# Performance work log

Measured on AMD Instinct MI355X. Metric: run time of the kernel, lower is better.

Reference implementation:

```python
import jax, jax.numpy as jnp
import numpy as np

B, E, D, T, R = 8192, 4096, 256, 128, 4
K = 64                # dkn_n_neighbors
TAU_SQ = 4.0          # tau**2
EMB_SCALE = 0.07      # keeps sq-dists ~2.5 so exp(-d2) weights are meaningful
LOG_BASE = -27.6310211159
EPS = 1e-12


def _rev_cumsum(a, axis):
    # flip -> cumsum -> flip, as in torch .flip().cumsum().flip()
    return jnp.flip(jnp.cumsum(jnp.flip(a, axis), axis), axis)


def _kernel_weights(x, ex):
    # exact KNN stand-in for the ANN index: squared L2 distances [B, E]
    d2 = (jnp.sum(x * x, axis=1, keepdims=True)
          + jnp.sum(ex * ex, axis=1)[None, :]
          - 2.0 * (x @ ex.T))
    neg_d2, idx = jax.lax.top_k(-d2, K)          # k nearest per query
    sq = jnp.maximum(-neg_d2, 0.0)               # [B, K]
    vals = jnp.exp(-sq) * (sq <= TAU_SQ).astype(x.dtype)
    rows = jnp.arange(x.shape[0])[:, None]       # [B, 1]
    # sparse exp-distance weights scattered into dense [B, E]
    return jnp.zeros((x.shape[0], ex.shape[0]), x.dtype).at[rows, idx].set(vals)


def setup_inputs() -> dict:
    key = jax.random.key(0)
    k0, k1, k2, k3 = jax.random.split(key, 4)
    x = jax.random.normal(k0, (B, D), dtype=jnp.float32) * EMB_SCALE
    ex = jax.random.normal(k1, (E, D), dtype=jnp.float32) * EMB_SCALE
    log_ev = jax.random.normal(k2, (E, T, R), dtype=jnp.float32) - 2.0
    log_cen = jax.random.normal(k3, (E, T), dtype=jnp.float32) - 2.0
    log_b_ev = jnp.full((T, R), LOG_BASE, dtype=jnp.float32)
    log_b_cen = jnp.full((T,), LOG_BASE, dtype=jnp.float32)
    return {
        "x": x,
        "exemplar_embeddings": ex,
        "log_exemplar_event_counts": log_ev,
        "log_exemplar_censor_counts": log_cen,
        "log_baseline_event_counts": log_b_ev,
        "log_baseline_censor_counts": log_b_cen,
    }


def reference(x, exemplar_embeddings, log_exemplar_event_counts,
              log_exemplar_censor_counts, log_baseline_event_counts,
              log_baseline_censor_counts):
    kw = _kernel_weights(x, exemplar_embeddings)             # [B, E]

    b_ev = jnp.exp(log_baseline_event_counts)                # [T, R]
    b_cen = jnp.exp(log_baseline_censor_counts)              # [T]
    b_at_risk = _rev_cumsum(b_ev.sum(1) + b_cen, 0)          # [T]

    ev = jnp.exp(log_exemplar_event_counts)                  # [E, T, R]
    cen = jnp.exp(log_exemplar_censor_counts)                # [E, T]
    at_risk = _rev_cumsum(ev.sum(2) + cen, 1)                # [E, T]

    denom = kw @ at_risk + b_at_risk[None, :] + EPS          # [B, T]
    numer = jnp.einsum('be,etr->btr', kw, ev) + b_ev[None]   # [B, T, R]

    esh = jnp.clip(numer / denom[..., None], EPS, 1.0 - EPS) # [B, T, R]
    event_specific_hazards = jnp.moveaxis(esh, -1, 0)        # [R, B, T]
    overall = jnp.clip(numer.sum(-1) / denom, EPS, 1.0 - EPS)  # [B, T]
    return event_specific_hazards, overall
```

## Files before the change

kernel.cpp:

```cpp
#include <hip/hip_runtime.h>
#include <hip/hip_fp16.h>
#include <math.h>

namespace {

constexpr int NB = 8192;
constexpr int NE = 4096;
constexpr int ND = 256;
constexpr int NT = 128;
constexpr int NR = 4;
constexpr int NK = 64;
constexpr int NCAND = 320;
constexpr float TAUSQ = 4.0f;
constexpr float FEPS = 1e-12f;
constexpr float QS = 256.0f / 4.5f;

typedef short s16x8 __attribute__((ext_vector_type(8)));
typedef float f32x4 __attribute__((ext_vector_type(4)));

__device__ __forceinline__ unsigned short f2bf_rne(float f) {
  unsigned int u = __float_as_uint(f);
  unsigned int r = (u + 0x7FFFu + ((u >> 16) & 1u)) >> 16;
  return (unsigned short)r;
}
__device__ __forceinline__ unsigned short f2h(float f) {
  return __half_as_ushort(__float2half(f));
}
__device__ __forceinline__ float h2f(unsigned short s) {
  return __half2float(__ushort_as_half(s));
}

__device__ __forceinline__ void gl_lds16(const void* g, void* lds) {
  __builtin_amdgcn_global_load_lds(
      (const __attribute__((address_space(1))) unsigned int*)g,
      (__attribute__((address_space(3))) unsigned int*)lds, 16, 0, 0);
}

__global__ void k_prep_base(const float* __restrict__ lbev, const float* __restrict__ lbcen,
                            float* __restrict__ bev, float* __restrict__ bar) {
  __shared__ float s[NT];
  int t = threadIdx.x;
  float acc = expf(lbcen[t]);
  for (int r = 0; r < NR; ++r) {
    float v = expf(lbev[t * NR + r]);
    bev[t * NR + r] = v;
    acc += v;
  }
  s[t] = acc;
  __syncthreads();
  float su = 0.f;
  for (int u = t; u < NT; ++u) su += s[u];
  bar[t] = su;
}

__global__ void k_prep_ev(const float* __restrict__ lev, const float* __restrict__ lcen,
                          unsigned short* __restrict__ EVh, unsigned short* __restrict__ ARh) {
  __shared__ float s[NT];
  int e = blockIdx.x, t = threadIdx.x;
  float acc = expf(lcen[(size_t)e * NT + t]);
  const float* src = lev + ((size_t)e * NT + t) * NR;
  float o0 = expf(src[0]), o1 = expf(src[1]), o2 = expf(src[2]), o3 = expf(src[3]);
  ushort4 h4;
  h4.x = f2h(o0); h4.y = f2h(o1); h4.z = f2h(o2); h4.w = f2h(o3);
  *reinterpret_cast<ushort4*>(EVh + ((size_t)e * NT + t) * NR) = h4;
  acc += o0 + o1 + o2 + o3;
  s[t] = acc;
  __syncthreads();
  float su = 0.f;
  for (int u = t; u < NT; ++u) su += s[u];
  ARh[(size_t)e * NT + t] = f2h(su);
}

__global__ void k_split(const float* __restrict__ x, const float* __restrict__ ex,
                        unsigned short* __restrict__ xh, unsigned short* __restrict__ eh,
                        float* __restrict__ xn, float* __restrict__ exn) {
  int row = blockIdx.x, l = threadIdx.x;
  bool isx = row < NB;
  const float* p = isx ? (x + (size_t)row * ND) : (ex + (size_t)(row - NB) * ND);
  unsigned short* dst = isx ? (xh + (size_t)row * ND) : (eh + (size_t)(row - NB) * ND);
  float4 v = reinterpret_cast<const float4*>(p)[l];
  float nv = v.x * v.x + v.y * v.y + v.z * v.z + v.w * v.w;
  ushort4 h4;
  h4.x = f2bf_rne(v.x); h4.y = f2bf_rne(v.y);
  h4.z = f2bf_rne(v.z); h4.w = f2bf_rne(v.w);
  reinterpret_cast<ushort4*>(dst)[l] = h4;
  for (int o = 32; o > 0; o >>= 1) nv += __shfl_down(nv, o);
  if (l == 0) { if (isx) xn[row] = nv; else exn[row - NB] = nv; }
}

__global__ __launch_bounds__(256) void k_dist_mfma(
    const unsigned short* __restrict__ xh, const unsigned short* __restrict__ eh,
    const float* __restrict__ xn, const float* __restrict__ exn,
    unsigned char* __restrict__ d2q) {
  __shared__ __align__(16) unsigned char As[128 * 64];
  __shared__ __align__(16) unsigned char Bs[128 * 64];
  int tid = threadIdx.x;
  int l = tid & 63, w = tid >> 6;
  int wr = w >> 1, wc = w & 1;
  int nb = blockIdx.x * 128, mb = blockIdx.y * 128;

  f32x4 acc[4][4];
  #pragma unroll
  for (int m = 0; m < 4; ++m)
    #pragma unroll
    for (int n = 0; n < 4; ++n)
      acc[m][n] = (f32x4){0.f, 0.f, 0.f, 0.f};

  for (int k0 = 0; k0 < ND; k0 += 32) {
    #pragma unroll
    for (int h = 0; h < 2; ++h) {
      int c = h * 256 + tid;
      int row = c >> 2, slot = c & 3;
      int swz = (row ^ (row >> 2)) & 3;
      int gcol = k0 + ((slot ^ swz) << 3);
      gl_lds16(xh + (size_t)(mb + row) * ND + gcol, As + c * 16);
      gl_lds16(eh + (size_t)(nb + row) * ND + gcol, Bs + c * 16);
    }
    __syncthreads();
    s16x8 af[4], bf_[4];
    int ko = l >> 4;
    #pragma unroll
    for (int m = 0; m < 4; ++m) {
      int r = wr * 64 + m * 16 + (l & 15);
      int swz = (r ^ (r >> 2)) & 3;
      af[m] = *(const s16x8*)(As + r * 64 + ((ko ^ swz) << 4));
    }
    #pragma unroll
    for (int n = 0; n < 4; ++n) {
      int r = wc * 64 + n * 16 + (l & 15);
      int swz = (r ^ (r >> 2)) & 3;
      bf_[n] = *(const s16x8*)(Bs + r * 64 + ((ko ^ swz) << 4));
    }
    #pragma unroll
    for (int m = 0; m < 4; ++m)
      #pragma unroll
      for (int n = 0; n < 4; ++n)
        acc[m][n] = __builtin_amdgcn_mfma_f32_16x16x32_bf16(af[m], bf_[n], acc[m][n], 0, 0, 0);
    __syncthreads();
  }

  int col0 = nb + wc * 64 + (l & 15);
  int row0 = mb + wr * 64 + (l >> 4) * 4;
  float exnv[4];
  #pragma unroll
  for (int n = 0; n < 4; ++n) exnv[n] = exn[col0 + n * 16];
  #pragma unroll
  for (int m = 0; m < 4; ++m) {
    #pragma unroll
    for (int j = 0; j < 4; ++j) {
      int qrow = row0 + m * 16 + j;
      float xq = xn[qrow];
      #pragma unroll
      for (int n = 0; n < 4; ++n) {
        float d2 = xq + exnv[n] - 2.f * acc[m][n][j];
        int bin = (int)floorf(d2 * QS);
        bin = bin < 0 ? 0 : (bin > 255 ? 255 : bin);
        d2q[(size_t)qrow * NE + (col0 + n * 16)] = (unsigned char)bin;
      }
    }
  }
}

__global__ __launch_bounds__(256, 8) void k_select(
    const unsigned char* __restrict__ d2q,
    const float* __restrict__ x, const float* __restrict__ ex,
    const float* __restrict__ xn, const float* __restrict__ exn,
    float* __restrict__ selw, int* __restrict__ seli) {
  __shared__ unsigned int hist[256];
  __shared__ float4 xs[64];
  __shared__ int cand_e[NCAND];
  __shared__ float cand_d[NCAND];
  __shared__ unsigned int wsum[4];
  __shared__ int s_cb, s_nc;

  int tid = threadIdx.x;
  int l = tid & 63, w = tid >> 6;
  int b = blockIdx.x;

  uint4 rb = reinterpret_cast<const uint4*>(d2q + (size_t)b * NE)[tid];
  if (tid < 64) xs[tid] = reinterpret_cast<const float4*>(x + (size_t)b * ND)[tid];
  hist[tid] = 0u;
  __syncthreads();

  unsigned int wd[4] = {rb.x, rb.y, rb.z, rb.w};
  #pragma unroll
  for (int c = 0; c < 4; ++c)
    #pragma unroll
    for (int k = 0; k < 4; ++k)
      atomicAdd(&hist[(wd[c] >> (8 * k)) & 255u], 1u);
  __syncthreads();

  if (w == 0) {
    unsigned int h0 = hist[l * 4], h1 = hist[l * 4 + 1], h2 = hist[l * 4 + 2], h3 = hist[l * 4 + 3];
    unsigned int gs = h0 + h1 + h2 + h3;
    unsigned int sc = gs;
    #pragma unroll
    for (int o = 1; o < 64; o <<= 1) { unsigned int v = __shfl_up(sc, o); if (l >= o) sc += v; }
    unsigned int excl = sc - gs;
    unsigned int c0 = excl + h0, c1 = c0 + h1, c2 = c1 + h2, c3 = c2 + h3;
    int local = (c0 >= (unsigned)NK) ? 0 : (c1 >= (unsigned)NK) ? 1
              : (c2 >= (unsigned)NK) ? 2 : (c3 >= (unsigned)NK) ? 3 : -1;
    unsigned long long ball = __ballot(local >= 0);
    int first = __ffsll((long long)ball) - 1;
    if (l == first) s_cb = l * 4 + local;
  }
  __syncthreads();
  int cbg = s_cb < 255 ? s_cb + 1 : 255;

  int myc = 0;
  #pragma unroll
  for (int c = 0; c < 4; ++c)
    #pragma unroll
    for (int k = 0; k < 4; ++k)
      myc += ((int)((wd[c] >> (8 * k)) & 255u) <= cbg) ? 1 : 0;
  int sc = myc;
  #pragma unroll
  for (int o = 1; o < 64; o <<= 1) { int v = __shfl_up(sc, o); if (l >= o) sc += v; }
  if (l == 63) wsum[w] = (unsigned)sc;
  __syncthreads();
  int base = 0;
  for (int i = 0; i < w; ++i) base += (int)wsum[i];
  int slot = base + sc - myc;
  #pragma unroll
  for (int c = 0; c < 4; ++c)
    #pragma unroll
    for (int k = 0; k < 4; ++k) {
      int bin = (int)((wd[c] >> (8 * k)) & 255u);
      if (bin <= cbg) {
        if (slot < NCAND) cand_e[slot] = tid * 16 + c * 4 + k;
        ++slot;
      }
    }
  if (tid == 255) s_nc = (base + sc) < NCAND ? (base + sc) : NCAND;
  __syncthreads();

  int nc = s_nc;
  float bxn = xn[b];
  int g = tid >> 4, gj = tid & 15;
  for (int c = g; c < nc; c += 16) {
    int e = cand_e[c];
    const float4* ep = reinterpret_cast<const float4*>(ex + (size_t)e * ND);
    float s = 0.f;
    #pragma unroll
    for (int it = 0; it < 4; ++it) {
      float4 xv = xs[gj + 16 * it];
      float4 evv = ep[gj + 16 * it];
      s += xv.x * evv.x + xv.y * evv.y + xv.z * evv.z + xv.w * evv.w;
    }
    s += __shfl_xor(s, 1, 16);
    s += __shfl_xor(s, 2, 16);
    s += __shfl_xor(s, 4, 16);
    s += __shfl_xor(s, 8, 16);
    if (gj == 0) cand_d[c] = bxn + exn[e] - 2.f * s;
  }
  __syncthreads();

  for (int i = tid; i < nc; i += 256) {
    float di = cand_d[i];
    int rank = 0;
    for (int j = 0; j < nc; ++j) {
      float dj = cand_d[j];
      rank += (dj < di) || (dj == di && j < i);
    }
    if (rank < NK) {
      float sq = fmaxf(di, 0.f);
      float wgt = (sq <= TAUSQ) ? expf(-sq) : 0.f;
      selw[(size_t)b * NK + rank] = wgt;
      seli[(size_t)b * NK + rank] = cand_e[i];
    }
  }
  if (tid >= nc && tid < NK) {
    selw[(size_t)b * NK + tid] = 0.f;
    seli[(size_t)b * NK + tid] = 0;
  }
}

__global__ __launch_bounds__(256) void k_out(
    const unsigned short* __restrict__ EVh, const unsigned short* __restrict__ ARh,
    const float* __restrict__ bev, const float* __restrict__ bar,
    const float* __restrict__ selw, const int* __restrict__ seli,
    float* __restrict__ out) {
  __shared__ float wl[NK];
  __shared__ int il[NK];
  __shared__ float snum[NT * NR];
  __shared__ float sden[NT];
  int tid = threadIdx.x;
  int b = blockIdx.x;
  if (tid < NK) { wl[tid] = selw[(size_t)b * NK + tid]; il[tid] = seli[(size_t)b * NK + tid]; }
  __syncthreads();

  int g = tid >> 7;
  int t = tid & 127;
  float acc0 = 0.f, acc1 = 0.f, acc2 = 0.f, acc3 = 0.f, dacc = 0.f;
  for (int k = g; k < NK; k += 2) {
    float wgt = wl[k];
    int e = il[k];
    ushort4 v = reinterpret_cast<const ushort4*>(EVh + (size_t)e * (NT * NR))[t];
    acc0 += wgt * h2f(v.x);
    acc1 += wgt * h2f(v.y);
    acc2 += wgt * h2f(v.z);
    acc3 += wgt * h2f(v.w);
    dacc += wgt * h2f(ARh[(size_t)e * NT + t]);
  }
  if (g == 0) {
    snum[t * 4 + 0] = acc0; snum[t * 4 + 1] = acc1;
    snum[t * 4 + 2] = acc2; snum[t * 4 + 3] = acc3;
    sden[t] = dacc;
  }
  __syncthreads();
  if (g == 1) {
    snum[t * 4 + 0] += acc0 + bev[t * 4 + 0];
    snum[t * 4 + 1] += acc1 + bev[t * 4 + 1];
    snum[t * 4 + 2] += acc2 + bev[t * 4 + 2];
    snum[t * 4 + 3] += acc3 + bev[t * 4 + 3];
    sden[t] += dacc + bar[t] + FEPS;
  }
  __syncthreads();

  const float lo = FEPS, hi = 1.0f - FEPS;
  {
    int f = tid;
    int tt = f >> 2, r = f & 3;
    float h = snum[f] / sden[tt];
    h = fminf(fmaxf(h, lo), hi);
    out[((size_t)r * NB + b) * NT + tt] = h;
    int f1 = tid + 256;
    int t1 = f1 >> 2, r1 = f1 & 3;
    float h1 = snum[f1] / sden[t1];
    h1 = fminf(fmaxf(h1, lo), hi);
    out[((size_t)r1 * NB + b) * NT + t1] = h1;
  }
  if (tid < NT) {
    float sum = snum[4 * tid] + snum[4 * tid + 1] + snum[4 * tid + 2] + snum[4 * tid + 3];
    float ov = sum / sden[tid];
    ov = fminf(fmaxf(ov, lo), hi);
    out[(size_t)4 * NB * NT + (size_t)b * NT + tid] = ov;
  }
}

}

extern "C" void kernel_launch(void* const* d_in, const int* in_sizes, int n_in,
                              void* d_out, int out_size, void* d_ws, size_t ws_size,
                              hipStream_t stream) {
  (void)in_sizes; (void)n_in; (void)out_size; (void)ws_size;
  const float* x     = (const float*)d_in[0];
  const float* ex    = (const float*)d_in[1];
  const float* lev   = (const float*)d_in[2];
  const float* lcen  = (const float*)d_in[3];
  const float* lbev  = (const float*)d_in[4];
  const float* lbcen = (const float*)d_in[5];
  float* out = (float*)d_out;

  char* ws = (char*)d_ws;
  unsigned short* EVh = (unsigned short*)(ws);
  unsigned short* ARh = (unsigned short*)(ws + (4ull << 20));
  float* bev = (float*)(ws + (5ull << 20));
  float* bar = (float*)(ws + (5ull << 20) + 4096);
  float* exn = (float*)(ws + (5ull << 20) + 8192);
  float* xn  = (float*)(ws + (5ull << 20) + 8192 + (16u << 10));
  unsigned char* d2q = (unsigned char*)(ws + (6ull << 20));
  float* selw = (float*)(ws + (38ull << 20));
  int*   seli = (int*)  (ws + (40ull << 20));
  unsigned short* xh = (unsigned short*)(ws + (42ull << 20));
  unsigned short* eh = (unsigned short*)(ws + (46ull << 20));

  k_prep_base<<<1, NT, 0, stream>>>(lbev, lbcen, bev, bar);
  k_prep_ev<<<NE, NT, 0, stream>>>(lev, lcen, EVh, ARh);
  k_split<<<NB + NE, 64, 0, stream>>>(x, ex, xh, eh, xn, exn);
  k_dist_mfma<<<dim3(NE / 128, NB / 128), 256, 0, stream>>>(xh, eh, xn, exn, d2q);
  k_select<<<NB, 256, 0, stream>>>(d2q, x, ex, xn, exn, selw, seli);
  k_out<<<NB, 256, 0, stream>>>(EVh, ARh, bev, bar, selw, seli, out);
}
```

Measured before the change: 235.2 us.

## Fuse prep kernels, widen GEMM K-tile, remap blocks, unroll candidate dot products

Merges the baseline and per-exemplar prep kernels into a single launch and replaces the quadratic suffix-sum loop with a wavefront shuffle scan. The distance GEMM now stages 64-wide K slices with an 8-way swizzle, halving the number of sync rounds, and remaps block IDs so that blocks likely to be resident together share data in cache. The candidate refinement loop keeps the query row in registers and handles two candidates per iteration to expose more memory parallelism. The larger LDS tiles may reduce occupancy, and the new scan and block remap have to match the reference exactly.

```diff
diff --git a/kernel.cpp b/kernel.cpp
--- a/kernel.cpp
+++ b/kernel.cpp
@@ -36,39 +36,41 @@
       (__attribute__((address_space(3))) unsigned int*)lds, 16, 0, 0);
 }
 
-__global__ void k_prep_base(const float* __restrict__ lbev, const float* __restrict__ lbcen,
-                            float* __restrict__ bev, float* __restrict__ bar) {
-  __shared__ float s[NT];
-  int t = threadIdx.x;
-  float acc = expf(lbcen[t]);
-  for (int r = 0; r < NR; ++r) {
-    float v = expf(lbev[t * NR + r]);
-    bev[t * NR + r] = v;
-    acc += v;
-  }
-  s[t] = acc;
-  __syncthreads();
-  float su = 0.f;
-  for (int u = t; u < NT; ++u) su += s[u];
-  bar[t] = su;
-}
-
-__global__ void k_prep_ev(const float* __restrict__ lev, const float* __restrict__ lcen,
-                          unsigned short* __restrict__ EVh, unsigned short* __restrict__ ARh) {
-  __shared__ float s[NT];
-  int e = blockIdx.x, t = threadIdx.x;
-  float acc = expf(lcen[(size_t)e * NT + t]);
-  const float* src = lev + ((size_t)e * NT + t) * NR;
-  float o0 = expf(src[0]), o1 = expf(src[1]), o2 = expf(src[2]), o3 = expf(src[3]);
-  ushort4 h4;
-  h4.x = f2h(o0); h4.y = f2h(o1); h4.z = f2h(o2); h4.w = f2h(o3);
-  *reinterpret_cast<ushort4*>(EVh + ((size_t)e * NT + t) * NR) = h4;
-  acc += o0 + o1 + o2 + o3;
-  s[t] = acc;
-  __syncthreads();
-  float su = 0.f;
-  for (int u = t; u < NT; ++u) su += s[u];
-  ARh[(size_t)e * NT + t] = f2h(su);
+__global__ void k_prep(const float* __restrict__ lev, const float* __restrict__ lcen,
+                       const float* __restrict__ lbev, const float* __restrict__ lbcen,
+                       unsigned short* __restrict__ EVh, unsigned short* __restrict__ ARh,
+                       float* __restrict__ bev, float* __restrict__ bar) {
+  __shared__ float wtot;
+  int t = threadIdx.x, l = t & 63;
+  int e = blockIdx.x;
+  float acc;
+  if (e < NE) {
+    acc = expf(lcen[(size_t)e * NT + t]);
+    const float* src = lev + ((size_t)e * NT + t) * NR;
+    float o0 = expf(src[0]), o1 = expf(src[1]), o2 = expf(src[2]), o3 = expf(src[3]);
+    ushort4 h4;
+    h4.x = f2h(o0); h4.y = f2h(o1); h4.z = f2h(o2); h4.w = f2h(o3);
+    *reinterpret_cast<ushort4*>(EVh + ((size_t)e * NT + t) * NR) = h4;
+    acc += o0 + o1 + o2 + o3;
+  } else {
+    acc = expf(lbcen[t]);
+    const float* src = lbev + t * NR;
+    float o0 = expf(src[0]), o1 = expf(src[1]), o2 = expf(src[2]), o3 = expf(src[3]);
+    bev[t * NR + 0] = o0; bev[t * NR + 1] = o1;
+    bev[t * NR + 2] = o2; bev[t * NR + 3] = o3;
+    acc += o0 + o1 + o2 + o3;
+  }
+  float v = acc;
+  #pragma unroll
+  for (int o = 1; o < 64; o <<= 1) {
+    float u = __shfl_down(v, o);
+    if (l + o < 64) v += u;
+  }
+  if (t == 64) wtot = v;
+  __syncthreads();
+  if (t < 64) v += wtot;
+  if (e < NE) ARh[(size_t)e * NT + t] = f2h(v);
+  else        bar[t] = v;
 }
 
 __global__ void k_split(const float* __restrict__ x, const float* __restrict__ ex,
@@ -92,12 +94,16 @@
     const unsigned short* __restrict__ xh, const unsigned short* __restrict__ eh,
     const float* __restrict__ xn, const float* __restrict__ exn,
     unsigned char* __restrict__ d2q) {
-  __shared__ __align__(16) unsigned char As[128 * 64];
-  __shared__ __align__(16) unsigned char Bs[128 * 64];
+  __shared__ __align__(16) unsigned char As[128 * 128];
+  __shared__ __align__(16) unsigned char Bs[128 * 128];
   int tid = threadIdx.x;
   int l = tid & 63, w = tid >> 6;
   int wr = w >> 1, wc = w & 1;
-  int nb = blockIdx.x * 128, mb = blockIdx.y * 128;
+
+  int lid = blockIdx.x;
+  int sl = (lid & 7) * 256 + (lid >> 3);
+  int nb = (sl & 31) * 128;
+  int mb = (sl >> 5) * 128;
 
   f32x4 acc[4][4];
   #pragma unroll
@@ -106,36 +112,39 @@
     for (int n = 0; n < 4; ++n)
       acc[m][n] = (f32x4){0.f, 0.f, 0.f, 0.f};
 
-  for (int k0 = 0; k0 < ND; k0 += 32) {
-    #pragma unroll
-    for (int h = 0; h < 2; ++h) {
+  for (int k0 = 0; k0 < ND; k0 += 64) {
+    #pragma unroll
+    for (int h = 0; h < 4; ++h) {
       int c = h * 256 + tid;
-      int row = c >> 2, slot = c & 3;
-      int swz = (row ^ (row >> 2)) & 3;
+      int row = c >> 3, slot = c & 7;
+      int swz = (row ^ (row >> 3)) & 7;
       int gcol = k0 + ((slot ^ swz) << 3);
       gl_lds16(xh + (size_t)(mb + row) * ND + gcol, As + c * 16);
       gl_lds16(eh + (size_t)(nb + row) * ND + gcol, Bs + c * 16);
     }
     __syncthreads();
-    s16x8 af[4], bf_[4];
-    int ko = l >> 4;
-    #pragma unroll
-    for (int m = 0; m < 4; ++m) {
-      int r = wr * 64 + m * 16 + (l & 15);
-      int swz = (r ^ (r >> 2)) & 3;
-      af[m] = *(const s16x8*)(As + r * 64 + ((ko ^ swz) << 4));
-    }
-    #pragma unroll
-    for (int n = 0; n < 4; ++n) {
-      int r = wc * 64 + n * 16 + (l & 15);
-      int swz = (r ^ (r >> 2)) & 3;
-      bf_[n] = *(const s16x8*)(Bs + r * 64 + ((ko ^ swz) << 4));
-    }
-    #pragma unroll
-    for (int m = 0; m < 4; ++m)
+    #pragma unroll
+    for (int kk = 0; kk < 2; ++kk) {
+      s16x8 af[4], bf_[4];
+      int sl0 = kk * 4 + (l >> 4);
       #pragma unroll
-      for (int n = 0; n < 4; ++n)
-        acc[m][n] = __builtin_amdgcn_mfma_f32_16x16x32_bf16(af[m], bf_[n], acc[m][n], 0, 0, 0);
+      for (int m = 0; m < 4; ++m) {
+        int r = wr * 64 + m * 16 + (l & 15);
+        int swz = (r ^ (r >> 3)) & 7;
+        af[m] = *(const s16x8*)(As + r * 128 + ((sl0 ^ swz) << 4));
+      }
+      #pragma unroll
+      for (int n = 0; n < 4; ++n) {
+        int r = wc * 64 + n * 16 + (l & 15);
+        int swz = (r ^ (r >> 3)) & 7;
+        bf_[n] = *(const s16x8*)(Bs + r * 128 + ((sl0 ^ swz) << 4));
+      }
+      #pragma unroll
+      for (int m = 0; m < 4; ++m)
+        #pragma unroll
+        for (int n = 0; n < 4; ++n)
+          acc[m][n] = __builtin_amdgcn_mfma_f32_16x16x32_bf16(af[m], bf_[n], acc[m][n], 0, 0, 0);
+    }
     __syncthreads();
   }
 
@@ -188,6 +197,9 @@
     #pragma unroll
     for (int k = 0; k < 4; ++k)
       atomicAdd(&hist[(wd[c] >> (8 * k)) & 255u], 1u);
+
+  int g = tid >> 4, gj = tid & 15;
+  float4 xr0 = xs[gj], xr1 = xs[gj + 16], xr2 = xs[gj + 32], xr3 = xs[gj + 48];
   __syncthreads();
 
   if (w == 0) {
@@ -236,22 +248,31 @@
 
   int nc = s_nc;
   float bxn = xn[b];
-  int g = tid >> 4, gj = tid & 15;
-  for (int c = g; c < nc; c += 16) {
-    int e = cand_e[c];
-    const float4* ep = reinterpret_cast<const float4*>(ex + (size_t)e * ND);
-    float s = 0.f;
-    #pragma unroll
-    for (int it = 0; it < 4; ++it) {
-      float4 xv = xs[gj + 16 * it];
-      float4 evv = ep[gj + 16 * it];
-      s += xv.x * evv.x + xv.y * evv.y + xv.z * evv.z + xv.w * evv.w;
-    }
-    s += __shfl_xor(s, 1, 16);
-    s += __shfl_xor(s, 2, 16);
-    s += __shfl_xor(s, 4, 16);
-    s += __shfl_xor(s, 8, 16);
-    if (gj == 0) cand_d[c] = bxn + exn[e] - 2.f * s;
+  for (int c = g; c < nc; c += 32) {
+    int eA = cand_e[c];
+    int has2 = (c + 16) < nc;
+    int eB = has2 ? cand_e[c + 16] : eA;
+    const float4* pA = reinterpret_cast<const float4*>(ex + (size_t)eA * ND);
+    const float4* pB = reinterpret_cast<const float4*>(ex + (size_t)eB * ND);
+    float4 a0 = pA[gj], a1 = pA[gj + 16], a2 = pA[gj + 32], a3 = pA[gj + 48];
+    float4 b0 = pB[gj], b1 = pB[gj + 16], b2 = pB[gj + 32], b3 = pB[gj + 48];
+    float sA = xr0.x * a0.x + xr0.y * a0.y + xr0.z * a0.z + xr0.w * a0.w
+             + xr1.x * a1.x + xr1.y * a1.y + xr1.z * a1.z + xr1.w * a1.w
+             + xr2.x * a2.x + xr2.y * a2.y + xr2.z * a2.z + xr2.w * a2.w
+             + xr3.x * a3.x + xr3.y * a3.y + xr3.z * a3.z + xr3.w * a3.w;
+    float sB = xr0.x * b0.x + xr0.y * b0.y + xr0.z * b0.z + xr0.w * b0.w
+             + xr1.x * b1.x + xr1.y * b1.y + xr1.z * b1.z + xr1.w * b1.w
+             + xr2.x * b2.x + xr2.y * b2.y + xr2.z * b2.z + xr2.w * b2.w
+             + xr3.x * b3.x + xr3.y * b3.y + xr3.z * b3.z + xr3.w * b3.w;
+    #pragma unroll
+    for (int o = 1; o < 16; o <<= 1) {
+      sA += __shfl_xor(sA, o, 16);
+      sB += __shfl_xor(sB, o, 16);
+    }
+    if (gj == 0) {
+      cand_d[c] = bxn + exn[eA] - 2.f * sA;
+      if (has2) cand_d[c + 16] = bxn + exn[eB] - 2.f * sB;
+    }
   }
   __syncthreads();
 
@@ -365,10 +386,9 @@
   unsigned short* xh = (unsigned short*)(ws + (42ull << 20));
   unsigned short* eh = (unsigned short*)(ws + (46ull << 20));
 
-  k_prep_base<<<1, NT, 0, stream>>>(lbev, lbcen, bev, bar);
-  k_prep_ev<<<NE, NT, 0, stream>>>(lev, lcen, EVh, ARh);
+  k_prep<<<NE + 1, NT, 0, stream>>>(lev, lcen, lbev, lbcen, EVh, ARh, bev, bar);
   k_split<<<NB + NE, 64, 0, stream>>>(x, ex, xh, eh, xn, exn);
-  k_dist_mfma<<<dim3(NE / 128, NB / 128), 256, 0, stream>>>(xh, eh, xn, exn, d2q);
+  k_dist_mfma<<<2048, 256, 0, stream>>>(xh, eh, xn, exn, d2q);
   k_select<<<NB, 256, 0, stream>>>(d2q, x, ex, xn, exn, selw, seli);
   k_out<<<NB, 256, 0, stream>>>(EVh, ARh, bev, bar, selw, seli, out);
 }
```

Result: faster. 213.0 us (-9.4%).
